# Kernel optimization log

Measured on AMD Instinct MI355X. Metric: run time of the kernel, lower is better.

Reference implementation:

```python
import jax, jax.numpy as jnp
import numpy as np

B = 65536
OBS_DIM = 85          # input_shape
FEAT = 8              # dim_entity_feature
NL = 5                # dim_landmarks
NT = 10               # dim_total
INF = 64              # in_features == out_features
HID = 64              # rnn_hidden_dim
NACT = 5              # n_actions
ALPHA = 0.01


def _leaky(x):
    return jnp.where(x > 0, x, ALPHA * x)


def setup_inputs() -> dict:
    key = jax.random.key(0)
    ks = jax.random.split(key, 26)
    s = 0.1
    d = {
        'obs': jax.random.normal(ks[0], (B, OBS_DIM), jnp.float32),
        'hidden_state': jax.random.normal(ks[1], (B, HID), jnp.float32),
        # entity input projections (input_layer_0/1/2), stored [in, out]
        'w_in0': jax.random.normal(ks[2], (FEAT, INF), jnp.float32) * s,
        'b_in0': jax.random.normal(ks[3], (INF,), jnp.float32) * s,
        'w_in1': jax.random.normal(ks[4], (FEAT, INF), jnp.float32) * s,
        'b_in1': jax.random.normal(ks[5], (INF,), jnp.float32) * s,
        'w_in2': jax.random.normal(ks[6], (FEAT, INF), jnp.float32) * s,
        'b_in2': jax.random.normal(ks[7], (INF,), jnp.float32) * s,
        # GAT params
        'W': jax.random.normal(ks[8], (INF, INF), jnp.float32) * s,
        'a': jax.random.normal(ks[9], (2 * INF, 1), jnp.float32) * s,
        # output MLP on attention rows (dim_soft = 2*dim_nearby = 10)
        'w_o1': jax.random.normal(ks[10], (2 * NL, 32), jnp.float32) * s,
        'b_o1': jax.random.normal(ks[11], (32,), jnp.float32) * s,
        'w_o2': jax.random.normal(ks[12], (32, 16), jnp.float32) * s,
        'b_o2': jax.random.normal(ks[13], (16,), jnp.float32) * s,
        'w_o3': jax.random.normal(ks[14], (16, 1), jnp.float32) * s,
        'b_o3': jax.random.normal(ks[15], (1,), jnp.float32) * s,
        # fc1 takes obs (85) concat atom_plug (5) -> 90
        'w_fc1': jax.random.normal(ks[16], (OBS_DIM + NL, HID), jnp.float32) * s,
        'b_fc1': jax.random.normal(ks[17], (HID,), jnp.float32) * s,
        # GRUCell, torch layout: [3H, in]
        'w_ih': jax.random.normal(ks[18], (3 * HID, HID), jnp.float32) * s,
        'w_hh': jax.random.normal(ks[19], (3 * HID, HID), jnp.float32) * s,
        'b_ih': jax.random.normal(ks[20], (3 * HID,), jnp.float32) * s,
        'b_hh': jax.random.normal(ks[21], (3 * HID,), jnp.float32) * s,
        'w_fc2': jax.random.normal(ks[22], (HID, NACT), jnp.float32) * s,
        'b_fc2': jax.random.normal(ks[23], (NACT,), jnp.float32) * s,
    }
    return d


def reference(obs, hidden_state, w_in0, b_in0, w_in1, b_in1, w_in2, b_in2,
              W, a, w_o1, b_o1, w_o2, b_o2, w_o3, b_o3,
              w_fc1, b_fc1, w_ih, w_hh, b_ih, b_hh, w_fc2, b_fc2):
    # data_preprocess: drop last dim_nearby cols, rotate first 4 to back, reshape to entities
    o = obs[:, :OBS_DIM - NL]                               # [B, 80]
    obs_in = jnp.concatenate([o[:, 4:], o[:, :4]], axis=-1).reshape(-1, NT, FEAT)  # [B,10,8]

    h0 = _leaky(obs_in @ w_in0 + b_in0)                     # [B,10,64]
    h1 = _leaky(obs_in @ w_in1 + b_in1)
    h2 = _leaky(obs_in @ w_in2 + b_in2)
    h_mix = jnp.concatenate([h0[:, :NL], h1[:, NL:NT - 1], h2[:, NT - 1:NT]], axis=1)  # [B,10,64]

    Wh = h_mix @ W                                          # [B,10,64]
    Wh1 = Wh @ a[:INF]                                      # [B,10,1]
    Wh2 = Wh @ a[INF:]                                      # [B,10,1]
    e = _leaky(Wh1 + jnp.swapaxes(Wh2, 1, 2))               # [B,10,10]

    att0 = jax.nn.softmax(e[:, :NL, NL:], axis=-1)          # [B,5,5]
    att1 = jnp.swapaxes(jax.nn.softmax(e[:, NL:, :NL], axis=-1), 1, 2)  # [B,5,5]
    attention = jnp.concatenate([att0, att1], axis=-1)      # [B,5,10]

    hp = _leaky(attention @ w_o1 + b_o1)
    hp = _leaky(hp @ w_o2 + b_o2)
    hp = _leaky(hp @ w_o3 + b_o3)[..., 0]                   # [B,5]
    obs_out = jax.nn.softmax(hp, axis=-1)                   # [B,5]

    obs_comb = jnp.concatenate([obs, obs_out], axis=-1)     # [B,90]
    x = jax.nn.relu(obs_comb @ w_fc1 + b_fc1)               # [B,64]

    h_in = hidden_state.reshape(-1, HID)
    gi = x @ w_ih.T + b_ih                                  # [B,192]
    gh = h_in @ w_hh.T + b_hh
    r = jax.nn.sigmoid(gi[:, :HID] + gh[:, :HID])
    z = jax.nn.sigmoid(gi[:, HID:2 * HID] + gh[:, HID:2 * HID])
    n = jnp.tanh(gi[:, 2 * HID:] + r * gh[:, 2 * HID:])
    h = (1.0 - z) * n + z * h_in                            # [B,64]

    q = h @ w_fc2 + b_fc2                                   # [B,5]
    return (q, h)
```

## Files before the change

### kernel.cpp

```cpp
#include <hip/hip_runtime.h>
#include <math.h>

namespace {

typedef __bf16 bf16x8 __attribute__((ext_vector_type(8)));
typedef float  f32x4  __attribute__((ext_vector_type(4)));
typedef float  f32x2  __attribute__((ext_vector_type(2)));

constexpr int B_      = 65536;
constexpr int OBS_DIM_= 85;
constexpr int NL_     = 5;
constexpr int NT_     = 10;
constexpr int HID_    = 64;
constexpr int NACT_   = 5;
constexpr float ALPHA_= 0.01f;

__device__ __forceinline__ float leaky(float x)    { return fmaf(fminf(x, 0.0f), ALPHA_ - 1.0f, x); }
__device__ __forceinline__ float sigmoidf(float x) { return 1.0f / (1.0f + __expf(-x)); }
__device__ __forceinline__ float tanh_fast(float x){ return 1.0f - 2.0f / (__expf(2.0f * x) + 1.0f); }

__global__ void prep_kernel(const float* __restrict__ W, const float* __restrict__ a,
                            const float* __restrict__ w_ih, const float* __restrict__ w_hh,
                            const float* __restrict__ w_fc1, void* __restrict__ ws) {
  float* Wa   = (float*)ws;
  __bf16* ih  = (__bf16*)((char*)ws + 512);
  __bf16* hh  = ih + 192 * 64;
  __bf16* f1t = hh + 192 * 64;
  const int tid = blockIdx.x * 256 + threadIdx.x;
  if (blockIdx.x == 0 && threadIdx.x < 64) {
    const int i = threadIdx.x;
    float s1 = 0.0f, s2 = 0.0f;
    #pragma unroll
    for (int j = 0; j < 64; ++j) {
      float w = W[i * 64 + j];
      s1 += w * a[j];
      s2 += w * a[64 + j];
    }
    Wa[i] = s1;
    Wa[64 + i] = s2;
  }
  const int stride = gridDim.x * 256;
  for (int i = tid; i < 192 * 64; i += stride) {
    int pr = i >> 6, k = i & 63;
    int g  = pr >> 6;
    int q  = pr & 63;
    int orig = (g << 6) + ((q & 15) << 2) + (q >> 4);
    ih[i] = (__bf16)w_ih[orig * 64 + k];
    hh[i] = (__bf16)w_hh[orig * 64 + k];
  }
  for (int i = tid; i < 64 * 96; i += stride) {
    int n = i / 96, k = i - 96 * n;
    f1t[i] = (__bf16)(k < 90 ? w_fc1[k * 64 + n] : 0.0f);
  }
}

__global__ __launch_bounds__(256) void front_kernel(
    const float* __restrict__ obs,
    const float* __restrict__ w_in0, const float* __restrict__ b_in0,
    const float* __restrict__ w_in1, const float* __restrict__ b_in1,
    const float* __restrict__ w_in2, const float* __restrict__ b_in2,
    const float* __restrict__ w_o1, const float* __restrict__ b_o1,
    const float* __restrict__ w_o2, const float* __restrict__ b_o2,
    const float* __restrict__ w_o3, const float* __restrict__ b_o3,
    const float* __restrict__ Wa,
    float* __restrict__ out5) {

  __shared__ __align__(16) float s_obs[16][84];
  __shared__ float s_wh1[16][12], s_wh2[16][12];
  __shared__ float s_colm[16][6], s_cols[16][6];
  __shared__ __align__(16) float s_att[16][5][12];
  __shared__ __align__(16) float s_h1[16][5][36];
  __shared__ __align__(16) float s_h2[16][5][20];
  __shared__ float s_hp[16][6];

  const int tid  = threadIdx.x;
  const int wv   = tid >> 6;
  const int lane = tid & 63;
  const int l16  = lane & 15;
  const int rloc = tid >> 4;
  const long gr0 = (long)blockIdx.x * 16;

  {
    const float* src = obs + (gr0 + wv * 4) * OBS_DIM_;
    #pragma unroll
    for (int c0 = 0; c0 < 5; ++c0) {
      int it = c0 * 64 + lane;
      int r = it / 80, c = it - 80 * r;
      s_obs[wv * 4 + r][c] = src[r * OBS_DIM_ + c];
    }
  }

  const int u0 = l16 * 4;
  const float* orow = s_obs[rloc];
  const f32x4 wa1 = *(const f32x4*)&Wa[u0];
  const f32x4 wa2 = *(const f32x4*)&Wa[64 + u0];

  f32x4 wA[8];
  #pragma unroll
  for (int f = 0; f < 8; ++f) wA[f] = *(const f32x4*)&w_in0[f * 64 + u0];
  f32x4 bA = *(const f32x4*)&b_in0[u0];

  #pragma unroll
  for (int t = 0; t < NT_; ++t) {
    if (t == 5) {
      #pragma unroll
      for (int f = 0; f < 8; ++f) wA[f] = *(const f32x4*)&w_in1[f * 64 + u0];
      bA = *(const f32x4*)&b_in1[u0];
    }
    if (t == 9) {
      #pragma unroll
      for (int f = 0; f < 8; ++f) wA[f] = *(const f32x4*)&w_in2[f * 64 + u0];
      bA = *(const f32x4*)&b_in2[u0];
    }
    const int ia = t * 8 + 4;
    int ib = t * 8 + 8;
    if (ib >= 80) ib = 0;
    f32x4 oa = *(const f32x4*)&orow[ia];
    f32x4 ob = *(const f32x4*)&orow[ib];
    f32x4 z = bA;
    #pragma unroll
    for (int f = 0; f < 4; ++f) {
      z[0] += oa[f] * wA[f][0]; z[1] += oa[f] * wA[f][1];
      z[2] += oa[f] * wA[f][2]; z[3] += oa[f] * wA[f][3];
    }
    #pragma unroll
    for (int f = 4; f < 8; ++f) {
      z[0] += ob[f - 4] * wA[f][0]; z[1] += ob[f - 4] * wA[f][1];
      z[2] += ob[f - 4] * wA[f][2]; z[3] += ob[f - 4] * wA[f][3];
    }
    float h0 = leaky(z[0]), h1 = leaky(z[1]), h2 = leaky(z[2]), h3 = leaky(z[3]);
    float p1t = h0 * wa1[0] + h1 * wa1[1] + h2 * wa1[2] + h3 * wa1[3];
    float p2t = h0 * wa2[0] + h1 * wa2[1] + h2 * wa2[2] + h3 * wa2[3];
    p1t += __shfl_xor(p1t, 1, 64);  p2t += __shfl_xor(p2t, 1, 64);
    p1t += __shfl_xor(p1t, 2, 64);  p2t += __shfl_xor(p2t, 2, 64);
    p1t += __shfl_xor(p1t, 4, 64);  p2t += __shfl_xor(p2t, 4, 64);
    p1t += __shfl_xor(p1t, 8, 64);  p2t += __shfl_xor(p2t, 8, 64);
    if (l16 == 0) { s_wh1[rloc][t] = p1t; s_wh2[rloc][t] = p2t; }
  }

  if (l16 >= 5 && l16 < 10) {
    const int jj = l16 - 5;
    float w1v = s_wh1[rloc][NL_ + jj];
    float ev[NL_], m = -1e30f;
    #pragma unroll
    for (int k = 0; k < NL_; ++k) { ev[k] = leaky(w1v + s_wh2[rloc][k]); m = fmaxf(m, ev[k]); }
    float s = 0.0f;
    #pragma unroll
    for (int k = 0; k < NL_; ++k) s += __expf(ev[k] - m);
    s_colm[rloc][jj] = m;
    s_cols[rloc][jj] = s;
  }

  if (l16 < NL_) {
    const int r = l16;
    const float wh1_r = s_wh1[rloc][r];
    const float wh2_r = s_wh2[rloc][r];
    float ev[NL_], m = -1e30f;
    #pragma unroll
    for (int j = 0; j < NL_; ++j) { ev[j] = leaky(wh1_r + s_wh2[rloc][NL_ + j]); m = fmaxf(m, ev[j]); }
    float a0[NL_], s = 0.0f;
    #pragma unroll
    for (int j = 0; j < NL_; ++j) { a0[j] = __expf(ev[j] - m); s += a0[j]; }
    float inv = 1.0f / s;
    #pragma unroll
    for (int j = 0; j < NL_; ++j) s_att[rloc][r][j] = a0[j] * inv;
    #pragma unroll
    for (int jj = 0; jj < NL_; ++jj) {
      float e = leaky(s_wh1[rloc][NL_ + jj] + wh2_r);
      s_att[rloc][r][NL_ + jj] = __expf(e - s_colm[rloc][jj]) / s_cols[rloc][jj];
    }
  }

  {
    f32x2 w1c[NT_];
    #pragma unroll
    for (int k = 0; k < NT_; ++k) w1c[k] = *(const f32x2*)&w_o1[k * 32 + l16 * 2];
    const f32x2 b1 = *(const f32x2*)&b_o1[l16 * 2];
    #pragma unroll
    for (int r5 = 0; r5 < NL_; ++r5) {
      float za = b1[0], zb = b1[1];
      #pragma unroll
      for (int k2 = 0; k2 < 5; ++k2) {
        f32x2 at = *(const f32x2*)&s_att[rloc][r5][k2 * 2];
        za += at[0] * w1c[2 * k2][0] + at[1] * w1c[2 * k2 + 1][0];
        zb += at[0] * w1c[2 * k2][1] + at[1] * w1c[2 * k2 + 1][1];
      }
      *(f32x2*)&s_h1[rloc][r5][l16 * 2] = f32x2{leaky(za), leaky(zb)};
    }
  }

  {
    float w2c[32];
    #pragma unroll
    for (int k = 0; k < 32; ++k) w2c[k] = w_o2[k * 16 + l16];
    const float b2 = b_o2[l16];
    #pragma unroll
    for (int r5 = 0; r5 < NL_; ++r5) {
      float z = b2;
      #pragma unroll
      for (int k4 = 0; k4 < 8; ++k4) {
        f32x4 hv = *(const f32x4*)&s_h1[rloc][r5][k4 * 4];
        z += hv[0] * w2c[4 * k4] + hv[1] * w2c[4 * k4 + 1]
           + hv[2] * w2c[4 * k4 + 2] + hv[3] * w2c[4 * k4 + 3];
      }
      s_h2[rloc][r5][l16] = leaky(z);
    }
  }

  if (l16 < NL_) {
    float z3 = b_o3[0];
    #pragma unroll
    for (int k4 = 0; k4 < 4; ++k4) {
      f32x4 hv = *(const f32x4*)&s_h2[rloc][l16][k4 * 4];
      z3 += hv[0] * w_o3[4 * k4] + hv[1] * w_o3[4 * k4 + 1]
          + hv[2] * w_o3[4 * k4 + 2] + hv[3] * w_o3[4 * k4 + 3];
    }
    float hp_own = leaky(z3);
    s_hp[rloc][l16] = hp_own;
    float m5 = -1e30f;
    #pragma unroll
    for (int j = 0; j < NL_; ++j) m5 = fmaxf(m5, s_hp[rloc][j]);
    float ssum = 0.0f;
    #pragma unroll
    for (int j = 0; j < NL_; ++j) ssum += __expf(s_hp[rloc][j] - m5);
    out5[(gr0 + rloc) * NL_ + l16] = __expf(hp_own - m5) / ssum;
  }
}

constexpr int ROWS_ = 64;
constexpr int SOB_  = 104;
constexpr int SXH_  = 72;

__global__ __launch_bounds__(256, 4) void gemm_kernel(
    const float* __restrict__ obs, const float* __restrict__ hidden,
    const float* __restrict__ b_fc1,
    const float* __restrict__ b_ih, const float* __restrict__ b_hh,
    const float* __restrict__ w_fc2, const float* __restrict__ b_fc2,
    const void* __restrict__ wsv,
    float* q5,
    float* __restrict__ h_out) {

  __shared__ __align__(16) __bf16 A_obs[ROWS_ * SOB_];
  __shared__ __align__(16) __bf16 A_x[ROWS_ * SXH_];

  const int tid  = threadIdx.x;
  const int wv   = tid >> 6;
  const int lane = tid & 63;
  const int l    = lane & 15;
  const int quad = lane >> 4;
  const int r0   = wv * 16;
  const long gr0 = (long)blockIdx.x * ROWS_;

  const __bf16* Wih = (const __bf16*)((const char*)wsv + 512);
  const __bf16* Whh = Wih + 192 * 64;
  const __bf16* Wf1 = Whh + 192 * 64;

  const float* src = obs + (gr0 + r0) * OBS_DIM_;
  f32x4 vobs[6];
  #pragma unroll
  for (int k = 0; k < 6; ++k) {
    int idx = lane + 64 * k;
    if (idx < 340) vobs[k] = *(const f32x4*)&src[idx * 4];
  }
  const float* o5 = q5 + (gr0 + r0) * NL_;
  float vo5a = o5[lane];
  float vo5b = (lane < 16) ? o5[lane + 64] : 0.0f;

  const float* hrow_g = hidden + (gr0 + r0 + l) * HID_;
  f32x4 vha0 = *(const f32x4*)&hrow_g[quad * 8];
  f32x4 vha1 = *(const f32x4*)&hrow_g[quad * 8 + 4];
  f32x4 vhb0 = *(const f32x4*)&hrow_g[32 + quad * 8];
  f32x4 vhb1 = *(const f32x4*)&hrow_g[32 + quad * 8 + 4];

  bf16x8 bf1[3][4];
  #pragma unroll
  for (int ks = 0; ks < 3; ++ks)
    #pragma unroll
    for (int nt = 0; nt < 4; ++nt)
      bf1[ks][nt] = *(const bf16x8*)&Wf1[(nt * 16 + l) * 96 + ks * 32 + quad * 8];

  #pragma unroll
  for (int k = 0; k < 6; ++k) {
    int idx = lane + 64 * k;
    if (idx < 340) {
      #pragma unroll
      for (int e = 0; e < 4; ++e) {
        int fe = idx * 4 + e;
        int rr = fe / 85, cc = fe - 85 * rr;
        A_obs[(r0 + rr) * SOB_ + cc] = (__bf16)vobs[k][e];
      }
    }
  }
  {
    int rr = lane / NL_, cc = lane - NL_ * rr;
    A_obs[(r0 + rr) * SOB_ + 85 + cc] = (__bf16)vo5a;
  }
  if (lane < 16) {
    int it = lane + 64;
    int rr = it / NL_, cc = it - NL_ * rr;
    A_obs[(r0 + rr) * SOB_ + 85 + cc] = (__bf16)vo5b;
  }
  #pragma unroll
  for (int p = 0; p < 2; ++p) {
    int it = lane + 64 * p;
    if (it < 96) {
      int rr = it / 6, cc = it - 6 * rr;
      A_obs[(r0 + rr) * SOB_ + 90 + cc] = (__bf16)0.0f;
    }
  }

  bf16x8 ah[2];
  {
    bf16x8 t;
    t[0] = (__bf16)vha0[0]; t[1] = (__bf16)vha0[1]; t[2] = (__bf16)vha0[2]; t[3] = (__bf16)vha0[3];
    t[4] = (__bf16)vha1[0]; t[5] = (__bf16)vha1[1]; t[6] = (__bf16)vha1[2]; t[7] = (__bf16)vha1[3];
    ah[0] = t;
    t[0] = (__bf16)vhb0[0]; t[1] = (__bf16)vhb0[1]; t[2] = (__bf16)vhb0[2]; t[3] = (__bf16)vhb0[3];
    t[4] = (__bf16)vhb1[0]; t[5] = (__bf16)vhb1[1]; t[6] = (__bf16)vhb1[2]; t[7] = (__bf16)vhb1[3];
    ah[1] = t;
  }

  const f32x4 zero4 = {0.0f, 0.0f, 0.0f, 0.0f};

  f32x4 cx[4];
  #pragma unroll
  for (int nt = 0; nt < 4; ++nt) cx[nt] = zero4;
  #pragma unroll
  for (int ks = 0; ks < 3; ++ks) {
    bf16x8 af = *(const bf16x8*)&A_obs[(r0 + l) * SOB_ + ks * 32 + quad * 8];
    #pragma unroll
    for (int nt = 0; nt < 4; ++nt)
      cx[nt] = __builtin_amdgcn_mfma_f32_16x16x32_bf16(af, bf1[ks][nt], cx[nt], 0, 0, 0);
  }
  #pragma unroll
  for (int nt = 0; nt < 4; ++nt) {
    float bias = b_fc1[nt * 16 + l];
    #pragma unroll
    for (int rg = 0; rg < 4; ++rg) {
      float xv = fmaxf(cx[nt][rg] + bias, 0.0f);
      A_x[(r0 + quad * 4 + rg) * SXH_ + nt * 16 + l] = (__bf16)xv;
    }
  }

  bf16x8 ax[2];
  #pragma unroll
  for (int ks = 0; ks < 2; ++ks)
    ax[ks] = *(const bf16x8*)&A_x[(r0 + l) * SXH_ + ks * 32 + quad * 8];

  f32x4 crz[8], cni[4], cnh[4];
  #pragma unroll
  for (int nt = 0; nt < 8; ++nt) crz[nt] = zero4;
  #pragma unroll
  for (int nt = 0; nt < 4; ++nt) { cni[nt] = zero4; cnh[nt] = zero4; }
  #pragma unroll
  for (int nt = 0; nt < 8; ++nt) {
    #pragma unroll
    for (int ks = 0; ks < 2; ++ks) {
      bf16x8 bi = *(const bf16x8*)&Wih[(nt * 16 + l) * 64 + ks * 32 + quad * 8];
      crz[nt] = __builtin_amdgcn_mfma_f32_16x16x32_bf16(ax[ks], bi, crz[nt], 0, 0, 0);
      bf16x8 bh = *(const bf16x8*)&Whh[(nt * 16 + l) * 64 + ks * 32 + quad * 8];
      crz[nt] = __builtin_amdgcn_mfma_f32_16x16x32_bf16(ah[ks], bh, crz[nt], 0, 0, 0);
    }
  }
  #pragma unroll
  for (int nt = 0; nt < 4; ++nt) {
    #pragma unroll
    for (int ks = 0; ks < 2; ++ks) {
      bf16x8 bi = *(const bf16x8*)&Wih[(128 + nt * 16 + l) * 64 + ks * 32 + quad * 8];
      cni[nt] = __builtin_amdgcn_mfma_f32_16x16x32_bf16(ax[ks], bi, cni[nt], 0, 0, 0);
      bf16x8 bh = *(const bf16x8*)&Whh[(128 + nt * 16 + l) * 64 + ks * 32 + quad * 8];
      cnh[nt] = __builtin_amdgcn_mfma_f32_16x16x32_bf16(ah[ks], bh, cnh[nt], 0, 0, 0);
    }
  }

  const long grow = gr0 + r0 + quad * 4;

  f32x4 br4, bz4, bin4, bhn4;
  {
    f32x4 a0 = *(const f32x4*)&b_ih[4 * l];
    f32x4 a1 = *(const f32x4*)&b_hh[4 * l];
    br4 = a0 + a1;
    a0 = *(const f32x4*)&b_ih[64 + 4 * l];
    a1 = *(const f32x4*)&b_hh[64 + 4 * l];
    bz4 = a0 + a1;
    bin4 = *(const f32x4*)&b_ih[128 + 4 * l];
    bhn4 = *(const f32x4*)&b_hh[128 + 4 * l];
  }
  f32x4 w20[5];
  #pragma unroll
  for (int j = 0; j < 5; ++j) w20[j] = *(const f32x4*)&w_fc2[20 * l + 4 * j];

  float qp[4][NACT_];
  #pragma unroll
  for (int rg = 0; rg < 4; ++rg)
    #pragma unroll
    for (int c = 0; c < NACT_; ++c) qp[rg][c] = 0.0f;

  #pragma unroll
  for (int rg = 0; rg < 4; ++rg) {
    f32x4 hold = *(const f32x4*)&hidden[(grow + rg) * HID_ + 4 * l];
    f32x4 hnew;
    #pragma unroll
    for (int t = 0; t < 4; ++t) {
      float rr = sigmoidf(crz[t][rg] + br4[t]);
      float zz = sigmoidf(crz[4 + t][rg] + bz4[t]);
      float nn = tanh_fast(cni[t][rg] + bin4[t] + rr * (cnh[t][rg] + bhn4[t]));
      float hn = (1.0f - zz) * nn + zz * hold[t];
      hnew[t] = hn;
      #pragma unroll
      for (int c = 0; c < NACT_; ++c)
        qp[rg][c] += hn * w20[(5 * t + c) >> 2][(5 * t + c) & 3];
    }
    *(f32x4*)&h_out[(grow + rg) * HID_ + 4 * l] = hnew;
  }

  #pragma unroll
  for (int m = 1; m < 16; m <<= 1) {
    #pragma unroll
    for (int rg = 0; rg < 4; ++rg)
      #pragma unroll
      for (int c = 0; c < NACT_; ++c) qp[rg][c] += __shfl_xor(qp[rg][c], m, 64);
  }
  if (l < NACT_) {
    #pragma unroll
    for (int rg = 0; rg < 4; ++rg) {
      float qv = qp[rg][0];
      if (l == 1) qv = qp[rg][1];
      if (l == 2) qv = qp[rg][2];
      if (l == 3) qv = qp[rg][3];
      if (l == 4) qv = qp[rg][4];
      q5[(grow + rg) * NACT_ + l] = qv + b_fc2[l];
    }
  }
}

}

extern "C" void kernel_launch(void* const* d_in, const int* in_sizes, int n_in,
                              void* d_out, int out_size, void* d_ws, size_t ws_size,
                              hipStream_t stream) {
  const float* obs    = (const float*)d_in[0];
  const float* hidden = (const float*)d_in[1];
  const float* w_in0  = (const float*)d_in[2];
  const float* b_in0  = (const float*)d_in[3];
  const float* w_in1  = (const float*)d_in[4];
  const float* b_in1  = (const float*)d_in[5];
  const float* w_in2  = (const float*)d_in[6];
  const float* b_in2  = (const float*)d_in[7];
  const float* W      = (const float*)d_in[8];
  const float* a      = (const float*)d_in[9];
  const float* w_o1   = (const float*)d_in[10];
  const float* b_o1   = (const float*)d_in[11];
  const float* w_o2   = (const float*)d_in[12];
  const float* b_o2   = (const float*)d_in[13];
  const float* w_o3   = (const float*)d_in[14];
  const float* b_o3   = (const float*)d_in[15];
  const float* w_fc1  = (const float*)d_in[16];
  const float* b_fc1  = (const float*)d_in[17];
  const float* w_ih   = (const float*)d_in[18];
  const float* w_hh   = (const float*)d_in[19];
  const float* b_ih   = (const float*)d_in[20];
  const float* b_hh   = (const float*)d_in[21];
  const float* w_fc2  = (const float*)d_in[22];
  const float* b_fc2  = (const float*)d_in[23];

  float* q_out = (float*)d_out;
  float* h_out = q_out + (long)B_ * NACT_;
  const float* Wa = (const float*)d_ws;

  prep_kernel<<<48, 256, 0, stream>>>(W, a, w_ih, w_hh, w_fc1, d_ws);
  front_kernel<<<B_ / 16, 256, 0, stream>>>(
      obs, w_in0, b_in0, w_in1, b_in1, w_in2, b_in2,
      w_o1, b_o1, w_o2, b_o2, w_o3, b_o3, Wa, q_out);
  gemm_kernel<<<B_ / ROWS_, 256, 0, stream>>>(
      obs, hidden, b_fc1, b_ih, b_hh, w_fc2, b_fc2, d_ws, q_out, h_out);
}
```

Baseline: 202.5 us.

## Fuse attention front kernel and GEMM/GRU kernel into one kernel

Merges the per-row attention front stage and the MFMA fc1/GRU stage into a single kernel handling 64 rows per block. The obs tile is staged into LDS once with global_load_lds, and the attention softmax output stays in shared memory instead of round-tripping through global memory. This removes a second read of obs, the intermediate out5 write/read, and one kernel launch. In exchange the block needs about 39 KB of LDS, overlapping buffers are aliased (A_x shares space with the attention scratch), and the attention MLP now runs in four serial passes per block. The hidden activations s_h1 are also stored as bf16.

```diff
diff --git a/kernel.cpp b/kernel.cpp
--- a/kernel.cpp
+++ b/kernel.cpp
@@ -4,8 +4,12 @@
 namespace {
 
 typedef __bf16 bf16x8 __attribute__((ext_vector_type(8)));
+typedef __bf16 bf16x4 __attribute__((ext_vector_type(4)));
 typedef float  f32x4  __attribute__((ext_vector_type(4)));
 typedef float  f32x2  __attribute__((ext_vector_type(2)));
+
+typedef __attribute__((address_space(1))) const char GChar;
+typedef __attribute__((address_space(3))) char LChar;
 
 constexpr int B_      = 65536;
 constexpr int OBS_DIM_= 85;
@@ -54,263 +58,220 @@
   }
 }
 
-__global__ __launch_bounds__(256) void front_kernel(
-    const float* __restrict__ obs,
+constexpr int SXH_ = 72;
+
+__global__ __launch_bounds__(256, 4) void fused_kernel(
+    const float* __restrict__ obs, const float* __restrict__ hidden,
     const float* __restrict__ w_in0, const float* __restrict__ b_in0,
     const float* __restrict__ w_in1, const float* __restrict__ b_in1,
     const float* __restrict__ w_in2, const float* __restrict__ b_in2,
     const float* __restrict__ w_o1, const float* __restrict__ b_o1,
     const float* __restrict__ w_o2, const float* __restrict__ b_o2,
     const float* __restrict__ w_o3, const float* __restrict__ b_o3,
-    const float* __restrict__ Wa,
-    float* __restrict__ out5) {
-
-  __shared__ __align__(16) float s_obs[16][84];
-  __shared__ float s_wh1[16][12], s_wh2[16][12];
-  __shared__ float s_colm[16][6], s_cols[16][6];
-  __shared__ __align__(16) float s_att[16][5][12];
-  __shared__ __align__(16) float s_h1[16][5][36];
-  __shared__ __align__(16) float s_h2[16][5][20];
-  __shared__ float s_hp[16][6];
+    const float* __restrict__ b_fc1,
+    const float* __restrict__ b_ih, const float* __restrict__ b_hh,
+    const float* __restrict__ w_fc2, const float* __restrict__ b_fc2,
+    const void* __restrict__ wsv,
+    float* __restrict__ q_out, float* __restrict__ h_out) {
+
+  __shared__ __align__(16) char smem[39168];
+  float* s_obs = (float*)smem;
+  float  (*s_att)[5][10] = (float (*)[5][10])(smem + 21760);
+  __bf16 (*s_h1)[5][32]  = (__bf16 (*)[5][32])(smem + 24960);
+  float  (*s_h2)[5][16]  = (float (*)[5][16])(smem + 30080);
+  __bf16* A_x            = (__bf16*)(smem + 21760);
+  float (*s_wh1)[12]     = (float (*)[12])(smem + 35200);
+  float (*s_wh2)[12]     = (float (*)[12])(smem + 35968);
+  float (*s_colm)[6]     = (float (*)[6])(smem + 36736);
+  float (*s_cols)[6]     = (float (*)[6])(smem + 37120);
+  float (*s_hp)[6]       = (float (*)[6])(smem + 37504);
+  float* s_o5            = (float*)(smem + 37888);
 
   const int tid  = threadIdx.x;
   const int wv   = tid >> 6;
   const int lane = tid & 63;
   const int l16  = lane & 15;
-  const int rloc = tid >> 4;
-  const long gr0 = (long)blockIdx.x * 16;
-
-  {
-    const float* src = obs + (gr0 + wv * 4) * OBS_DIM_;
-    #pragma unroll
-    for (int c0 = 0; c0 < 5; ++c0) {
-      int it = c0 * 64 + lane;
-      int r = it / 80, c = it - 80 * r;
-      s_obs[wv * 4 + r][c] = src[r * OBS_DIM_ + c];
-    }
-  }
-
-  const int u0 = l16 * 4;
-  const float* orow = s_obs[rloc];
-  const f32x4 wa1 = *(const f32x4*)&Wa[u0];
-  const f32x4 wa2 = *(const f32x4*)&Wa[64 + u0];
-
-  f32x4 wA[8];
-  #pragma unroll
-  for (int f = 0; f < 8; ++f) wA[f] = *(const f32x4*)&w_in0[f * 64 + u0];
-  f32x4 bA = *(const f32x4*)&b_in0[u0];
-
-  #pragma unroll
-  for (int t = 0; t < NT_; ++t) {
-    if (t == 5) {
-      #pragma unroll
-      for (int f = 0; f < 8; ++f) wA[f] = *(const f32x4*)&w_in1[f * 64 + u0];
-      bA = *(const f32x4*)&b_in1[u0];
-    }
-    if (t == 9) {
-      #pragma unroll
-      for (int f = 0; f < 8; ++f) wA[f] = *(const f32x4*)&w_in2[f * 64 + u0];
-      bA = *(const f32x4*)&b_in2[u0];
-    }
-    const int ia = t * 8 + 4;
-    int ib = t * 8 + 8;
-    if (ib >= 80) ib = 0;
-    f32x4 oa = *(const f32x4*)&orow[ia];
-    f32x4 ob = *(const f32x4*)&orow[ib];
-    f32x4 z = bA;
-    #pragma unroll
-    for (int f = 0; f < 4; ++f) {
-      z[0] += oa[f] * wA[f][0]; z[1] += oa[f] * wA[f][1];
-      z[2] += oa[f] * wA[f][2]; z[3] += oa[f] * wA[f][3];
-    }
-    #pragma unroll
-    for (int f = 4; f < 8; ++f) {
-      z[0] += ob[f - 4] * wA[f][0]; z[1] += ob[f - 4] * wA[f][1];
-      z[2] += ob[f - 4] * wA[f][2]; z[3] += ob[f - 4] * wA[f][3];
-    }
-    float h0 = leaky(z[0]), h1 = leaky(z[1]), h2 = leaky(z[2]), h3 = leaky(z[3]);
-    float p1t = h0 * wa1[0] + h1 * wa1[1] + h2 * wa1[2] + h3 * wa1[3];
-    float p2t = h0 * wa2[0] + h1 * wa2[1] + h2 * wa2[2] + h3 * wa2[3];
-    p1t += __shfl_xor(p1t, 1, 64);  p2t += __shfl_xor(p2t, 1, 64);
-    p1t += __shfl_xor(p1t, 2, 64);  p2t += __shfl_xor(p2t, 2, 64);
-    p1t += __shfl_xor(p1t, 4, 64);  p2t += __shfl_xor(p2t, 4, 64);
-    p1t += __shfl_xor(p1t, 8, 64);  p2t += __shfl_xor(p2t, 8, 64);
-    if (l16 == 0) { s_wh1[rloc][t] = p1t; s_wh2[rloc][t] = p2t; }
-  }
-
-  if (l16 >= 5 && l16 < 10) {
-    const int jj = l16 - 5;
-    float w1v = s_wh1[rloc][NL_ + jj];
-    float ev[NL_], m = -1e30f;
-    #pragma unroll
-    for (int k = 0; k < NL_; ++k) { ev[k] = leaky(w1v + s_wh2[rloc][k]); m = fmaxf(m, ev[k]); }
-    float s = 0.0f;
-    #pragma unroll
-    for (int k = 0; k < NL_; ++k) s += __expf(ev[k] - m);
-    s_colm[rloc][jj] = m;
-    s_cols[rloc][jj] = s;
-  }
-
-  if (l16 < NL_) {
-    const int r = l16;
-    const float wh1_r = s_wh1[rloc][r];
-    const float wh2_r = s_wh2[rloc][r];
-    float ev[NL_], m = -1e30f;
-    #pragma unroll
-    for (int j = 0; j < NL_; ++j) { ev[j] = leaky(wh1_r + s_wh2[rloc][NL_ + j]); m = fmaxf(m, ev[j]); }
-    float a0[NL_], s = 0.0f;
-    #pragma unroll
-    for (int j = 0; j < NL_; ++j) { a0[j] = __expf(ev[j] - m); s += a0[j]; }
-    float inv = 1.0f / s;
-    #pragma unroll
-    for (int j = 0; j < NL_; ++j) s_att[rloc][r][j] = a0[j] * inv;
-    #pragma unroll
-    for (int jj = 0; jj < NL_; ++jj) {
-      float e = leaky(s_wh1[rloc][NL_ + jj] + wh2_r);
-      s_att[rloc][r][NL_ + jj] = __expf(e - s_colm[rloc][jj]) / s_cols[rloc][jj];
-    }
-  }
-
-  {
-    f32x2 w1c[NT_];
-    #pragma unroll
-    for (int k = 0; k < NT_; ++k) w1c[k] = *(const f32x2*)&w_o1[k * 32 + l16 * 2];
-    const f32x2 b1 = *(const f32x2*)&b_o1[l16 * 2];
-    #pragma unroll
-    for (int r5 = 0; r5 < NL_; ++r5) {
-      float za = b1[0], zb = b1[1];
-      #pragma unroll
-      for (int k2 = 0; k2 < 5; ++k2) {
-        f32x2 at = *(const f32x2*)&s_att[rloc][r5][k2 * 2];
-        za += at[0] * w1c[2 * k2][0] + at[1] * w1c[2 * k2 + 1][0];
-        zb += at[0] * w1c[2 * k2][1] + at[1] * w1c[2 * k2 + 1][1];
-      }
-      *(f32x2*)&s_h1[rloc][r5][l16 * 2] = f32x2{leaky(za), leaky(zb)};
-    }
-  }
-
-  {
-    float w2c[32];
-    #pragma unroll
-    for (int k = 0; k < 32; ++k) w2c[k] = w_o2[k * 16 + l16];
-    const float b2 = b_o2[l16];
-    #pragma unroll
-    for (int r5 = 0; r5 < NL_; ++r5) {
-      float z = b2;
-      #pragma unroll
-      for (int k4 = 0; k4 < 8; ++k4) {
-        f32x4 hv = *(const f32x4*)&s_h1[rloc][r5][k4 * 4];
-        z += hv[0] * w2c[4 * k4] + hv[1] * w2c[4 * k4 + 1]
-           + hv[2] * w2c[4 * k4 + 2] + hv[3] * w2c[4 * k4 + 3];
-      }
-      s_h2[rloc][r5][l16] = leaky(z);
-    }
-  }
-
-  if (l16 < NL_) {
-    float z3 = b_o3[0];
-    #pragma unroll
-    for (int k4 = 0; k4 < 4; ++k4) {
-      f32x4 hv = *(const f32x4*)&s_h2[rloc][l16][k4 * 4];
-      z3 += hv[0] * w_o3[4 * k4] + hv[1] * w_o3[4 * k4 + 1]
-          + hv[2] * w_o3[4 * k4 + 2] + hv[3] * w_o3[4 * k4 + 3];
-    }
-    float hp_own = leaky(z3);
-    s_hp[rloc][l16] = hp_own;
-    float m5 = -1e30f;
-    #pragma unroll
-    for (int j = 0; j < NL_; ++j) m5 = fmaxf(m5, s_hp[rloc][j]);
-    float ssum = 0.0f;
-    #pragma unroll
-    for (int j = 0; j < NL_; ++j) ssum += __expf(s_hp[rloc][j] - m5);
-    out5[(gr0 + rloc) * NL_ + l16] = __expf(hp_own - m5) / ssum;
-  }
-}
-
-constexpr int ROWS_ = 64;
-constexpr int SOB_  = 104;
-constexpr int SXH_  = 72;
-
-__global__ __launch_bounds__(256, 4) void gemm_kernel(
-    const float* __restrict__ obs, const float* __restrict__ hidden,
-    const float* __restrict__ b_fc1,
-    const float* __restrict__ b_ih, const float* __restrict__ b_hh,
-    const float* __restrict__ w_fc2, const float* __restrict__ b_fc2,
-    const void* __restrict__ wsv,
-    float* q5,
-    float* __restrict__ h_out) {
-
-  __shared__ __align__(16) __bf16 A_obs[ROWS_ * SOB_];
-  __shared__ __align__(16) __bf16 A_x[ROWS_ * SXH_];
-
-  const int tid  = threadIdx.x;
-  const int wv   = tid >> 6;
-  const int lane = tid & 63;
-  const int l    = lane & 15;
-  const int quad = lane >> 4;
-  const int r0   = wv * 16;
-  const long gr0 = (long)blockIdx.x * ROWS_;
-
+  const int grp  = tid >> 4;
+  const long gr0 = (long)blockIdx.x * 64;
+
+  const float* Wa = (const float*)wsv;
   const __bf16* Wih = (const __bf16*)((const char*)wsv + 512);
   const __bf16* Whh = Wih + 192 * 64;
   const __bf16* Wf1 = Whh + 192 * 64;
 
-  const float* src = obs + (gr0 + r0) * OBS_DIM_;
-  f32x4 vobs[6];
-  #pragma unroll
-  for (int k = 0; k < 6; ++k) {
-    int idx = lane + 64 * k;
-    if (idx < 340) vobs[k] = *(const f32x4*)&src[idx * 4];
-  }
-  const float* o5 = q5 + (gr0 + r0) * NL_;
-  float vo5a = o5[lane];
-  float vo5b = (lane < 16) ? o5[lane + 64] : 0.0f;
-
-  const float* hrow_g = hidden + (gr0 + r0 + l) * HID_;
-  f32x4 vha0 = *(const f32x4*)&hrow_g[quad * 8];
-  f32x4 vha1 = *(const f32x4*)&hrow_g[quad * 8 + 4];
-  f32x4 vhb0 = *(const f32x4*)&hrow_g[32 + quad * 8];
-  f32x4 vhb1 = *(const f32x4*)&hrow_g[32 + quad * 8 + 4];
-
-  bf16x8 bf1[3][4];
-  #pragma unroll
-  for (int ks = 0; ks < 3; ++ks)
-    #pragma unroll
-    for (int nt = 0; nt < 4; ++nt)
-      bf1[ks][nt] = *(const bf16x8*)&Wf1[(nt * 16 + l) * 96 + ks * 32 + quad * 8];
-
-  #pragma unroll
-  for (int k = 0; k < 6; ++k) {
-    int idx = lane + 64 * k;
-    if (idx < 340) {
-      #pragma unroll
-      for (int e = 0; e < 4; ++e) {
-        int fe = idx * 4 + e;
-        int rr = fe / 85, cc = fe - 85 * rr;
-        A_obs[(r0 + rr) * SOB_ + cc] = (__bf16)vobs[k][e];
-      }
-    }
-  }
   {
-    int rr = lane / NL_, cc = lane - NL_ * rr;
-    A_obs[(r0 + rr) * SOB_ + 85 + cc] = (__bf16)vo5a;
-  }
-  if (lane < 16) {
-    int it = lane + 64;
-    int rr = it / NL_, cc = it - NL_ * rr;
-    A_obs[(r0 + rr) * SOB_ + 85 + cc] = (__bf16)vo5b;
-  }
-  #pragma unroll
-  for (int p = 0; p < 2; ++p) {
-    int it = lane + 64 * p;
-    if (it < 96) {
-      int rr = it / 6, cc = it - 6 * rr;
-      A_obs[(r0 + rr) * SOB_ + 90 + cc] = (__bf16)0.0f;
-    }
-  }
+    const char* gbase = (const char*)(obs + gr0 * OBS_DIM_) + wv * 5440;
+    char* lbase = smem + wv * 5440;
+    #pragma unroll
+    for (int j = 0; j < 5; ++j)
+      __builtin_amdgcn_global_load_lds((const GChar*)(gbase + j * 1024 + lane * 16),
+                                       (LChar*)(lbase + j * 1024 + lane * 16), 16, 0, 0);
+    if (lane < 20)
+      __builtin_amdgcn_global_load_lds((const GChar*)(gbase + 5120 + lane * 16),
+                                       (LChar*)(lbase + 5120 + lane * 16), 16, 0, 0);
+  }
+
+  const int u0 = l16 * 4;
+  const f32x4 wa1 = *(const f32x4*)&Wa[u0];
+  const f32x4 wa2 = *(const f32x4*)&Wa[64 + u0];
+
+  asm volatile("s_waitcnt vmcnt(0)" ::: "memory");
+  __syncthreads();
+
+  #pragma unroll 1
+  for (int pass = 0; pass < 4; ++pass) {
+    const int row = pass * 16 + grp;
+    const float* orow = s_obs + row * OBS_DIM_;
+
+    f32x4 wA[8];
+    f32x4 bA;
+    #pragma unroll
+    for (int t = 0; t < NT_; ++t) {
+      if (t == 0) {
+        #pragma unroll
+        for (int f = 0; f < 8; ++f) wA[f] = *(const f32x4*)&w_in0[f * 64 + u0];
+        bA = *(const f32x4*)&b_in0[u0];
+      }
+      if (t == 5) {
+        #pragma unroll
+        for (int f = 0; f < 8; ++f) wA[f] = *(const f32x4*)&w_in1[f * 64 + u0];
+        bA = *(const f32x4*)&b_in1[u0];
+      }
+      if (t == 9) {
+        #pragma unroll
+        for (int f = 0; f < 8; ++f) wA[f] = *(const f32x4*)&w_in2[f * 64 + u0];
+        bA = *(const f32x4*)&b_in2[u0];
+      }
+      const int ia = t * 8 + 4;
+      int ib = t * 8 + 8;
+      if (ib >= 80) ib = 0;
+      float oa[4], ob[4];
+      #pragma unroll
+      for (int e = 0; e < 4; ++e) { oa[e] = orow[ia + e]; ob[e] = orow[ib + e]; }
+      f32x4 z = bA;
+      #pragma unroll
+      for (int f = 0; f < 4; ++f) {
+        z[0] += oa[f] * wA[f][0]; z[1] += oa[f] * wA[f][1];
+        z[2] += oa[f] * wA[f][2]; z[3] += oa[f] * wA[f][3];
+      }
+      #pragma unroll
+      for (int f = 4; f < 8; ++f) {
+        z[0] += ob[f - 4] * wA[f][0]; z[1] += ob[f - 4] * wA[f][1];
+        z[2] += ob[f - 4] * wA[f][2]; z[3] += ob[f - 4] * wA[f][3];
+      }
+      float h0 = leaky(z[0]), h1 = leaky(z[1]), h2 = leaky(z[2]), h3 = leaky(z[3]);
+      float p1t = h0 * wa1[0] + h1 * wa1[1] + h2 * wa1[2] + h3 * wa1[3];
+      float p2t = h0 * wa2[0] + h1 * wa2[1] + h2 * wa2[2] + h3 * wa2[3];
+      p1t += __shfl_xor(p1t, 1, 64);  p2t += __shfl_xor(p2t, 1, 64);
+      p1t += __shfl_xor(p1t, 2, 64);  p2t += __shfl_xor(p2t, 2, 64);
+      p1t += __shfl_xor(p1t, 4, 64);  p2t += __shfl_xor(p2t, 4, 64);
+      p1t += __shfl_xor(p1t, 8, 64);  p2t += __shfl_xor(p2t, 8, 64);
+      if (l16 == 0) { s_wh1[grp][t] = p1t; s_wh2[grp][t] = p2t; }
+    }
+
+    if (l16 >= 5 && l16 < 10) {
+      const int jj = l16 - 5;
+      float w1v = s_wh1[grp][NL_ + jj];
+      float ev[NL_], m = -1e30f;
+      #pragma unroll
+      for (int k = 0; k < NL_; ++k) { ev[k] = leaky(w1v + s_wh2[grp][k]); m = fmaxf(m, ev[k]); }
+      float s = 0.0f;
+      #pragma unroll
+      for (int k = 0; k < NL_; ++k) s += __expf(ev[k] - m);
+      s_colm[grp][jj] = m;
+      s_cols[grp][jj] = s;
+    }
+
+    if (l16 < NL_) {
+      const int r = l16;
+      const float wh1_r = s_wh1[grp][r];
+      const float wh2_r = s_wh2[grp][r];
+      float ev[NL_], m = -1e30f;
+      #pragma unroll
+      for (int j = 0; j < NL_; ++j) { ev[j] = leaky(wh1_r + s_wh2[grp][NL_ + j]); m = fmaxf(m, ev[j]); }
+      float a0[NL_], s = 0.0f;
+      #pragma unroll
+      for (int j = 0; j < NL_; ++j) { a0[j] = __expf(ev[j] - m); s += a0[j]; }
+      float inv = 1.0f / s;
+      #pragma unroll
+      for (int j = 0; j < NL_; ++j) s_att[grp][r][j] = a0[j] * inv;
+      #pragma unroll
+      for (int jj = 0; jj < NL_; ++jj) {
+        float e = leaky(s_wh1[grp][NL_ + jj] + wh2_r);
+        s_att[grp][r][NL_ + jj] = __expf(e - s_colm[grp][jj]) / s_cols[grp][jj];
+      }
+    }
+
+    {
+      f32x2 w1c[NT_];
+      #pragma unroll
+      for (int k = 0; k < NT_; ++k) w1c[k] = *(const f32x2*)&w_o1[k * 32 + l16 * 2];
+      const f32x2 b1 = *(const f32x2*)&b_o1[l16 * 2];
+      #pragma unroll
+      for (int r5 = 0; r5 < NL_; ++r5) {
+        float za = b1[0], zb = b1[1];
+        #pragma unroll
+        for (int k2 = 0; k2 < 5; ++k2) {
+          f32x2 at = *(const f32x2*)&s_att[grp][r5][k2 * 2];
+          za += at[0] * w1c[2 * k2][0] + at[1] * w1c[2 * k2 + 1][0];
+          zb += at[0] * w1c[2 * k2][1] + at[1] * w1c[2 * k2 + 1][1];
+        }
+        s_h1[grp][r5][l16 * 2]     = (__bf16)leaky(za);
+        s_h1[grp][r5][l16 * 2 + 1] = (__bf16)leaky(zb);
+      }
+    }
+
+    {
+      float w2c[32];
+      #pragma unroll
+      for (int k = 0; k < 32; ++k) w2c[k] = w_o2[k * 16 + l16];
+      const float b2 = b_o2[l16];
+      #pragma unroll
+      for (int r5 = 0; r5 < NL_; ++r5) {
+        float z = b2;
+        #pragma unroll
+        for (int k4 = 0; k4 < 8; ++k4) {
+          bf16x4 hv = *(const bf16x4*)&s_h1[grp][r5][k4 * 4];
+          z += (float)hv[0] * w2c[4 * k4] + (float)hv[1] * w2c[4 * k4 + 1]
+             + (float)hv[2] * w2c[4 * k4 + 2] + (float)hv[3] * w2c[4 * k4 + 3];
+        }
+        s_h2[grp][r5][l16] = leaky(z);
+      }
+    }
+
+    if (l16 < NL_) {
+      float z3 = b_o3[0];
+      #pragma unroll
+      for (int k4 = 0; k4 < 4; ++k4) {
+        f32x4 hv = *(const f32x4*)&s_h2[grp][l16][k4 * 4];
+        z3 += hv[0] * w_o3[4 * k4] + hv[1] * w_o3[4 * k4 + 1]
+            + hv[2] * w_o3[4 * k4 + 2] + hv[3] * w_o3[4 * k4 + 3];
+      }
+      float hp_own = leaky(z3);
+      s_hp[grp][l16] = hp_own;
+      float m5 = -1e30f;
+      #pragma unroll
+      for (int j = 0; j < NL_; ++j) m5 = fmaxf(m5, s_hp[grp][j]);
+      float ssum = 0.0f;
+      #pragma unroll
+      for (int j = 0; j < NL_; ++j) ssum += __expf(s_hp[grp][j] - m5);
+      s_o5[row * NL_ + l16] = __expf(hp_own - m5) / ssum;
+    }
+  }
+
+  __syncthreads();
+
+  const int l    = l16;
+  const int quad = lane >> 4;
+  const int r0   = wv * 16;
 
   bf16x8 ah[2];
   {
+    const float* hrow_g = hidden + (gr0 + r0 + l) * HID_;
+    f32x4 vha0 = *(const f32x4*)&hrow_g[quad * 8];
+    f32x4 vha1 = *(const f32x4*)&hrow_g[quad * 8 + 4];
+    f32x4 vhb0 = *(const f32x4*)&hrow_g[32 + quad * 8];
+    f32x4 vhb1 = *(const f32x4*)&hrow_g[32 + quad * 8 + 4];
     bf16x8 t;
     t[0] = (__bf16)vha0[0]; t[1] = (__bf16)vha0[1]; t[2] = (__bf16)vha0[2]; t[3] = (__bf16)vha0[3];
     t[4] = (__bf16)vha1[0]; t[5] = (__bf16)vha1[1]; t[6] = (__bf16)vha1[2]; t[7] = (__bf16)vha1[3];
@@ -320,14 +281,44 @@
     ah[1] = t;
   }
 
+  bf16x8 bf1[3][4];
+  #pragma unroll
+  for (int ks = 0; ks < 3; ++ks)
+    #pragma unroll
+    for (int nt = 0; nt < 4; ++nt)
+      bf1[ks][nt] = *(const bf16x8*)&Wf1[(nt * 16 + l) * 96 + ks * 32 + quad * 8];
+
   const f32x4 zero4 = {0.0f, 0.0f, 0.0f, 0.0f};
+  const float* myrow = s_obs + (r0 + l) * OBS_DIM_;
+  const float* myo5  = s_o5 + (r0 + l) * NL_;
 
   f32x4 cx[4];
   #pragma unroll
   for (int nt = 0; nt < 4; ++nt) cx[nt] = zero4;
   #pragma unroll
   for (int ks = 0; ks < 3; ++ks) {
-    bf16x8 af = *(const bf16x8*)&A_obs[(r0 + l) * SOB_ + ks * 32 + quad * 8];
+    bf16x8 af;
+    if (ks < 2) {
+      const int cb = ks * 32 + quad * 8;
+      #pragma unroll
+      for (int j = 0; j < 8; ++j) af[j] = (__bf16)myrow[cb + j];
+    } else {
+      if (quad < 2) {
+        const int cb = 64 + quad * 8;
+        #pragma unroll
+        for (int j = 0; j < 8; ++j) af[j] = (__bf16)myrow[cb + j];
+      } else if (quad == 2) {
+        #pragma unroll
+        for (int j = 0; j < 5; ++j) af[j] = (__bf16)myrow[80 + j];
+        #pragma unroll
+        for (int j = 5; j < 8; ++j) af[j] = (__bf16)myo5[j - 5];
+      } else {
+        af[0] = (__bf16)myo5[3];
+        af[1] = (__bf16)myo5[4];
+        #pragma unroll
+        for (int j = 2; j < 8; ++j) af[j] = (__bf16)0.0f;
+      }
+    }
     #pragma unroll
     for (int nt = 0; nt < 4; ++nt)
       cx[nt] = __builtin_amdgcn_mfma_f32_16x16x32_bf16(af, bf1[ks][nt], cx[nt], 0, 0, 0);
@@ -429,7 +420,7 @@
       if (l == 2) qv = qp[rg][2];
       if (l == 3) qv = qp[rg][3];
       if (l == 4) qv = qp[rg][4];
-      q5[(grow + rg) * NACT_ + l] = qv + b_fc2[l];
+      q_out[(grow + rg) * NACT_ + l] = qv + b_fc2[l];
     }
   }
 }
@@ -466,12 +457,12 @@
 
   float* q_out = (float*)d_out;
   float* h_out = q_out + (long)B_ * NACT_;
-  const float* Wa = (const float*)d_ws;
 
   prep_kernel<<<48, 256, 0, stream>>>(W, a, w_ih, w_hh, w_fc1, d_ws);
-  front_kernel<<<B_ / 16, 256, 0, stream>>>(
-      obs, w_in0, b_in0, w_in1, b_in1, w_in2, b_in2,
-      w_o1, b_o1, w_o2, b_o2, w_o3, b_o3, Wa, q_out);
-  gemm_kernel<<<B_ / ROWS_, 256, 0, stream>>>(
-      obs, hidden, b_fc1, b_ih, b_hh, w_fc2, b_fc2, d_ws, q_out, h_out);
+  fused_kernel<<<B_ / 64, 256, 0, stream>>>(
+      obs, hidden,
+      w_in0, b_in0, w_in1, b_in1, w_in2, b_in2,
+      w_o1, b_o1, w_o2, b_o2, w_o3, b_o3,
+      b_fc1, b_ih, b_hh, w_fc2, b_fc2,
+      d_ws, q_out, h_out);
 }
```

Result: slower. 277.7 us (+37.1%).
